# Kernel optimization log

Hardware: AMD Instinct MI355X
Metric: run time of the kernel (lower is better)

The kernel has to match this reference:

```python
import jax, jax.numpy as jnp
import numpy as np

N_WIRES = 16
VAR_DEPTH = 2
BATCH = 16


def _param_sizes():
    sizes = []
    n = N_WIRES
    lay = 0
    while n > 1:
        sizes.append(4 * int(np.ceil(N_WIRES / 2 ** lay)) * VAR_DEPTH)
        n = (n + 1) // 2
        lay += 1
    return sizes  # [128, 64, 32, 16]


def _apply_1q(psi, gate, w):
    # psi: (B, 2, ..., 2); gate: (2,2) complex; wire w lives on axis w+1
    psi = jnp.moveaxis(psi, w + 1, -1)
    psi = jnp.einsum('...j,ij->...i', psi, gate)
    return jnp.moveaxis(psi, -1, w + 1)


def _rx(psi, th, w):
    c = jnp.cos(th / 2).astype(jnp.complex64)
    s = jnp.sin(th / 2).astype(jnp.complex64)
    gate = jnp.stack([jnp.stack([c, -1j * s]), jnp.stack([-1j * s, c])])
    return _apply_1q(psi, gate, w)


def _rz(psi, th, w):
    ph = jnp.exp(0.5j * th * jnp.array([-1.0, 1.0], jnp.float32)).astype(jnp.complex64)
    shape = [1] * psi.ndim
    shape[w + 1] = 2
    return psi * ph.reshape(shape)


def _rzz(psi, th, wa, wb):
    # diag(e^{-i t/2}, e^{i t/2}, e^{i t/2}, e^{-i t/2}) -> sign = -1 if bits equal else +1
    sgn = jnp.array([[-1.0, 1.0], [1.0, -1.0]], jnp.float32)
    ph = jnp.exp(0.5j * th * sgn).astype(jnp.complex64)  # symmetric, transpose-safe
    a, b = min(wa, wb) + 1, max(wa, wb) + 1
    shape = [1] * psi.ndim
    shape[a] = 2
    shape[b] = 2
    return psi * ph.reshape(shape)


def _cnot(psi, c, t):
    p0 = jax.lax.slice_in_dim(psi, 0, 1, axis=c + 1)
    p1 = jax.lax.slice_in_dim(psi, 1, 2, axis=c + 1)
    return jnp.concatenate([p0, jnp.flip(p1, axis=t + 1)], axis=c + 1)


def _conv_layer(psi, params, active):
    n = len(active)
    for d in range(VAR_DEPTH):
        for j in range(n):
            base = 4 * j + d * 4 * n
            psi = _rx(psi, params[base + 0], active[j])
            psi = _rz(psi, params[base + 1], active[j])
            psi = _rx(psi, params[base + 2], active[j])
        for bg in (0, 1):
            for j in range(bg, n, 2):
                jn = (j + 1) % n  # ring coupling (wraps last->first)
                base = 4 * j + d * 4 * n
                psi = _rzz(psi, params[base + 3], active[j], active[jn])
    return psi


def _pool(psi, active):
    for j in range(0, len(active), 2):
        if j + 1 < len(active):
            psi = _cnot(psi, active[j], active[j + 1])
    return psi, active[::2]


def _forward(psi, params_list):
    active = list(range(N_WIRES))
    for p in params_list:
        psi = _conv_layer(psi, p, active)
        if len(active) > 1:
            psi, active = _pool(psi, active)
    w = active[0]  # measure Z on the surviving wire (wire 0)
    prob = psi.real ** 2 + psi.imag ** 2
    axes = tuple(a for a in range(1, psi.ndim) if a != w + 1)
    p2 = prob.sum(axis=axes)  # (B, 2)
    return p2[:, 0] - p2[:, 1]


def setup_inputs() -> dict:
    key = jax.random.key(0)
    ks = jax.random.split(key, 8)
    dim = 2 ** N_WIRES
    x_re = jax.random.normal(ks[0], (BATCH, dim), dtype=jnp.float32)
    x_im = jax.random.normal(ks[1], (BATCH, dim), dtype=jnp.float32)
    nrm = jnp.sqrt(jnp.sum(x_re ** 2 + x_im ** 2, axis=1, keepdims=True))
    x_re = x_re / nrm
    x_im = x_im / nrm
    sizes = _param_sizes()
    two_pi = 2.0 * np.pi
    params = [jax.random.uniform(ks[2 + i], (sizes[i],), dtype=jnp.float32) * two_pi
              for i in range(len(sizes))]
    return {"x_re": x_re, "x_im": x_im,
            "params0": params[0], "params1": params[1],
            "params2": params[2], "params3": params[3]}


def reference(x_re, x_im, params0, params1, params2, params3):
    psi = (x_re + 1j * x_im).astype(jnp.complex64)
    psi = psi.reshape((BATCH,) + (2,) * N_WIRES)
    return _forward(psi, [params0, params1, params2, params3])
```

## Files before the change

### kernel.cpp

```cpp
#include <hip/hip_runtime.h>


#define DEV __device__ __forceinline__
#define TBL(i) (tbl + (i)*8)

__device__ static const unsigned char G_CP[60] = {
  15,14,13,12,11,10,9,8,7,6,5,4,3,2,1,0,
  15,14,13,12,11,10,9,8,7,6,5,4,3,2,1,0,
  15,13,11,9,7,5,3,1,
  15,13,11,9,7,5,3,1,
  15,11,7,3,
  15,11,7,3,
  15,7,
  15,7
};
__device__ static const unsigned char G_CQ[60] = {
  14,13,12,11,10,9,8,7,6,5,4,3,2,1,0,15,
  14,13,12,11,10,9,8,7,6,5,4,3,2,1,0,15,
  13,11,9,7,5,3,1,15,
  13,11,9,7,5,3,1,15,
  11,7,3,15,
  11,7,3,15,
  7,15,
  7,15
};

DEV float2 F2(float x, float y){ float2 r; r.x = x; r.y = y; return r; }
DEV float2 cmulf(float2 a, float2 b){ return F2(a.x*b.x - a.y*b.y, a.x*b.y + a.y*b.x); }
DEV int swz(int j){ return j ^ ((j>>4)&15) ^ ((j>>8)&15); }

template<int A,int B>
DEV int mapj(int t, int s){
  int j = ((s&1)<<A) | (((s>>1)&1)<<B);
  int ti = 0;
  #pragma unroll
  for (int b=0;b<11;b++){
    if (b!=A && b!=B){ j |= ((t>>ti)&1)<<b; ti++; }
  }
  return j;
}

template<int SB>
DEV void gate4(float2* a, const float* __restrict__ g){
  float u00r=g[0],u00i=g[1],u01r=g[2],u01i=g[3],u10r=g[4],u10i=g[5],u11r=g[6],u11i=g[7];
  #pragma unroll
  for (int m=0;m<2;m++){
    int i0 = (SB==0) ? (m<<1) : m;
    int i1 = i0 | (1<<SB);
    float2 x0=a[i0], x1=a[i1];
    a[i0] = F2(u00r*x0.x - u00i*x0.y + u01r*x1.x - u01i*x1.y,
               u00r*x0.y + u00i*x0.x + u01r*x1.y + u01i*x1.x);
    a[i1] = F2(u10r*x0.x - u10i*x0.y + u11r*x1.x - u11i*x1.y,
               u10r*x0.y + u10i*x0.x + u11r*x1.y + u11i*x1.x);
  }
}

template<int C0,int N,unsigned M0,unsigned M1>
DEV void diag4(float2* a, const float* __restrict__ tbl, unsigned Ib){
  const unsigned regmask = M0|M1;
  float2 F0 = F2(1.f, 0.f);
  #pragma unroll
  for (int k=0;k<N;k++){
    const int p = G_CP[C0+k], q = G_CQ[C0+k];
    if ( !(((1u<<p)|(1u<<q)) & regmask) ){
      float c = tbl[480 + 2*(C0+k)], s = tbl[481 + 2*(C0+k)];
      unsigned x = ((Ib>>p) ^ (Ib>>q)) & 1u;
      F0 = cmulf(F0, F2(c, x ? s : -s));
    }
  }
  #pragma unroll
  for (int r=0;r<4;r++){
    unsigned Ir = Ib ^ ((r&1)?M0:0u) ^ ((r&2)?M1:0u);
    float2 ph = F0;
    #pragma unroll
    for (int k=0;k<N;k++){
      const int p = G_CP[C0+k], q = G_CQ[C0+k];
      if ( ((1u<<p)|(1u<<q)) & regmask ){
        float c = tbl[480 + 2*(C0+k)], s = tbl[481 + 2*(C0+k)];
        unsigned x = ((Ir>>p) ^ (Ir>>q)) & 1u;
        ph = cmulf(ph, F2(c, x ? s : -s));
      }
    }
    a[r] = cmulf(a[r], ph);
  }
}

DEV unsigned Ia(int j, int o){ return (unsigned)(j | (o<<11)); }
DEV unsigned Ib2(int j, int o){ return (unsigned)((j&63) | (o<<6) | ((j>>6)<<11)); }
DEV unsigned Ic(int j, int o){
  return (unsigned)( ((j&1)<<1) | (((j>>1)&1)<<3) | (((j>>2)&1)<<5)
       | (((j>>3)&63)<<6) | (((j>>9)&1)<<13) | (((j>>10)&1)<<15)
       | (o&1) | (((o>>1)&1)<<2) | (((o>>2)&1)<<4) | (((o>>3)&1)<<12) | (((o>>4)&1)<<14) );
}
DEV int s2perm(int j){ return j ^ (((j>>8)&1)<<6) ^ (((j>>4)&1)<<2) ^ (((j>>1)&1)<<0); }
DEV int s3perm(int j){ return j ^ (((j>>10)&1)<<8) ^ (((j>>4)&1)<<1); }

__global__ void k_setup(const float* __restrict__ p0, const float* __restrict__ p1,
                        const float* __restrict__ p2, const float* __restrict__ p3,
                        float* __restrict__ tbl, float* __restrict__ out){
  int g = threadIdx.x;
  if (g < 16) out[g] = 0.f;
  if (g >= 60) return;
  int d, j, n; const float* P;
  if (g < 32)      { n=16; d=(g>>4)&1; j=g&15; P=p0; }
  else if (g < 48) { n=8;  d=(g>>3)&1; j=g&7;  P=p1; }
  else if (g < 56) { n=4;  d=(g>>2)&1; j=g&3;  P=p2; }
  else             { n=2;  d=(g>>1)&1; j=g&1;  P=p3; }
  int base = 4*j + 4*n*d;
  double th0 = P[base+0], th1 = P[base+1], th2 = P[base+2], th3 = P[base+3];
  double c0 = cos(th0*0.5), s0 = sin(th0*0.5);
  double ca = cos(th1*0.5), sa = sin(th1*0.5);
  double c2 = cos(th2*0.5), s2 = sin(th2*0.5);
  double B00r =  ca*c0, B00i = -sa*c0;
  double B01r = -sa*s0, B01i = -ca*s0;
  double B10r =  sa*s0, B10i = -ca*s0;
  double B11r =  ca*c0, B11i =  sa*c0;
  float* o = tbl + g*8;
  o[0]=(float)(c2*B00r + s2*B10i); o[1]=(float)(c2*B00i - s2*B10r);
  o[2]=(float)(c2*B01r + s2*B11i); o[3]=(float)(c2*B01i - s2*B11r);
  o[4]=(float)(s2*B00i + c2*B10r); o[5]=(float)(-s2*B00r + c2*B10i);
  o[6]=(float)(s2*B01i + c2*B11r); o[7]=(float)(-s2*B01r + c2*B11i);
  tbl[480 + 2*g] = (float)cos(th3*0.5);
  tbl[481 + 2*g] = (float)sin(th3*0.5);
}

__global__ __launch_bounds__(512, 4)
void k_p1(const float* __restrict__ xre, const float* __restrict__ xim,
          const float* __restrict__ tbl, float2* __restrict__ st){
  const int t = threadIdx.x;
  const int batch = blockIdx.x >> 5, o = blockIdx.x & 31;
  const unsigned hi = ((unsigned)batch<<16) | ((unsigned)o<<11);
  __shared__ float2 lds[2][2048];
  float2 a[4];
  {
    unsigned base = hi | ((unsigned)t<<2);
    float4 re = *(const float4*)(xre + base);
    float4 im = *(const float4*)(xim + base);
    a[0]=F2(re.x,im.x); a[1]=F2(re.y,im.y); a[2]=F2(re.z,im.z); a[3]=F2(re.w,im.w);
  }
  gate4<0>(a, TBL(15)); gate4<1>(a, TBL(14));
  #pragma unroll
  for (int s=0;s<4;s++) lds[0][swz(mapj<0,1>(t,s))] = a[s];
  __syncthreads();
  #pragma unroll
  for (int s=0;s<4;s++) a[s] = lds[0][swz(mapj<2,3>(t,s))];
  gate4<0>(a, TBL(13)); gate4<1>(a, TBL(12));
  #pragma unroll
  for (int s=0;s<4;s++) lds[1][swz(mapj<2,3>(t,s))] = a[s];
  __syncthreads();
  #pragma unroll
  for (int s=0;s<4;s++) a[s] = lds[1][swz(mapj<4,5>(t,s))];
  gate4<0>(a, TBL(11)); gate4<1>(a, TBL(10));
  #pragma unroll
  for (int s=0;s<4;s++) lds[0][swz(mapj<4,5>(t,s))] = a[s];
  __syncthreads();
  #pragma unroll
  for (int s=0;s<4;s++) a[s] = lds[0][swz(mapj<6,7>(t,s))];
  gate4<0>(a, TBL(9)); gate4<1>(a, TBL(8));
  #pragma unroll
  for (int s=0;s<4;s++) lds[1][swz(mapj<6,7>(t,s))] = a[s];
  __syncthreads();
  #pragma unroll
  for (int s=0;s<4;s++) a[s] = lds[1][swz(mapj<8,9>(t,s))];
  gate4<0>(a, TBL(7)); gate4<1>(a, TBL(6));
  #pragma unroll
  for (int s=0;s<4;s++) lds[0][swz(mapj<8,9>(t,s))] = a[s];
  __syncthreads();
  #pragma unroll
  for (int s=0;s<4;s++) a[s] = lds[0][swz(mapj<0,10>(t,s))];
  gate4<1>(a, TBL(5));
  #pragma unroll
  for (int s=0;s<4;s++) st[hi | (unsigned)mapj<0,10>(t,s)] = a[s];
}

__global__ __launch_bounds__(512, 4)
void k_p2(const float* __restrict__ tbl, float2* __restrict__ st){
  const int t = threadIdx.x;
  const int batch = blockIdx.x >> 5, o = blockIdx.x & 31;
  const unsigned bb = (unsigned)batch<<16;
  __shared__ float2 lds[2][2048];
  float2 a[4];
  #pragma unroll
  for (int s=0;s<4;s++) a[s] = st[bb | Ib2(mapj<10,9>(t,s), o)];
  gate4<0>(a, TBL(0)); gate4<1>(a, TBL(1));
  #pragma unroll
  for (int s=0;s<4;s++) lds[0][swz(mapj<10,9>(t,s))] = a[s];
  __syncthreads();
  #pragma unroll
  for (int s=0;s<4;s++) a[s] = lds[0][swz(mapj<8,7>(t,s))];
  gate4<0>(a, TBL(2)); gate4<1>(a, TBL(3));
  #pragma unroll
  for (int s=0;s<4;s++) lds[1][swz(mapj<8,7>(t,s))] = a[s];
  __syncthreads();
  #pragma unroll
  for (int s=0;s<4;s++) a[s] = lds[1][swz(mapj<6,5>(t,s))];
  gate4<0>(a, TBL(4));
  diag4<0,16, (1u<<11),(1u<<5)>(a, tbl, Ib2(mapj<6,5>(t,0), o));
  gate4<0>(a, TBL(20)); gate4<1>(a, TBL(26));
  #pragma unroll
  for (int s=0;s<4;s++) lds[0][swz(mapj<6,5>(t,s))] = a[s];
  __syncthreads();
  #pragma unroll
  for (int s=0;s<4;s++) a[s] = lds[0][swz(mapj<7,8>(t,s))];
  gate4<0>(a, TBL(19)); gate4<1>(a, TBL(18));
  #pragma unroll
  for (int s=0;s<4;s++) lds[1][swz(mapj<7,8>(t,s))] = a[s];
  __syncthreads();
  #pragma unroll
  for (int s=0;s<4;s++) a[s] = lds[1][swz(mapj<9,10>(t,s))];
  gate4<0>(a, TBL(17)); gate4<1>(a, TBL(16));
  #pragma unroll
  for (int s=0;s<4;s++) lds[0][swz(mapj<9,10>(t,s))] = a[s];
  __syncthreads();
  #pragma unroll
  for (int s=0;s<4;s++) a[s] = lds[0][swz(mapj<0,1>(t,s))];
  gate4<0>(a, TBL(31)); gate4<1>(a, TBL(30));
  #pragma unroll
  for (int s=0;s<4;s++) lds[1][swz(mapj<0,1>(t,s))] = a[s];
  __syncthreads();
  #pragma unroll
  for (int s=0;s<4;s++) a[s] = lds[1][swz(mapj<2,3>(t,s))];
  gate4<0>(a, TBL(29)); gate4<1>(a, TBL(28));
  #pragma unroll
  for (int s=0;s<4;s++) lds[0][swz(mapj<2,3>(t,s))] = a[s];
  __syncthreads();
  #pragma unroll
  for (int s=0;s<4;s++) a[s] = lds[0][swz(mapj<4,10>(t,s))];
  gate4<0>(a, TBL(27));
  #pragma unroll
  for (int s=0;s<4;s++) st[bb | Ib2(mapj<4,10>(t,s), o)] = a[s];
}

__global__ __launch_bounds__(512, 4)
void k_p3(const float* __restrict__ tbl, float2* __restrict__ st){
  const int t = threadIdx.x;
  const int batch = blockIdx.x >> 5, o = blockIdx.x & 31;
  const unsigned hi = ((unsigned)batch<<16) | ((unsigned)o<<11);
  __shared__ float2 lds[2][2048];
  float2 a[4];
  #pragma unroll
  for (int s=0;s<4;s++) a[s] = st[hi | (unsigned)mapj<6,7>(t,s)];
  gate4<0>(a, TBL(25)); gate4<1>(a, TBL(24));
  #pragma unroll
  for (int s=0;s<4;s++) lds[0][swz(mapj<6,7>(t,s))] = a[s];
  __syncthreads();
  #pragma unroll
  for (int s=0;s<4;s++) a[s] = lds[0][swz(mapj<8,9>(t,s))];
  gate4<0>(a, TBL(23)); gate4<1>(a, TBL(22));
  #pragma unroll
  for (int s=0;s<4;s++) lds[1][swz(mapj<8,9>(t,s))] = a[s];
  __syncthreads();
  #pragma unroll
  for (int s=0;s<4;s++) a[s] = lds[1][swz(mapj<0,10>(t,s))];
  gate4<1>(a, TBL(21));
  diag4<16,16, 1u,(1u<<10)>(a, tbl, Ia(mapj<0,10>(t,0), o));
  #pragma unroll
  for (int s=0;s<4;s++) st[hi | (unsigned)mapj<0,10>(t,s)] = a[s];
}

__global__ __launch_bounds__(512, 4)
void k_p4(const float* __restrict__ tbl, float2* __restrict__ st, float* __restrict__ out){
  const int t = threadIdx.x;
  const int batch = blockIdx.x >> 5, o = blockIdx.x & 31;
  const unsigned bb = (unsigned)batch<<16;
  __shared__ float2 lds[2][2048];
  __shared__ float red[8];
  float2 a[4];
  #pragma unroll
  for (int s=0;s<4;s++){
    unsigned I = Ic(mapj<10,9>(t,s), o);
    I ^= (I & 0xAAAAu) >> 1;
    a[s] = st[bb | I];
  }
  gate4<0>(a, TBL(32)); gate4<1>(a, TBL(33));
  #pragma unroll
  for (int s=0;s<4;s++) lds[0][swz(mapj<10,9>(t,s))] = a[s];
  __syncthreads();
  #pragma unroll
  for (int s=0;s<4;s++) a[s] = lds[0][swz(mapj<8,6>(t,s))];
  gate4<0>(a, TBL(34)); gate4<1>(a, TBL(35));
  #pragma unroll
  for (int s=0;s<4;s++) lds[1][swz(mapj<8,6>(t,s))] = a[s];
  __syncthreads();
  #pragma unroll
  for (int s=0;s<4;s++) a[s] = lds[1][swz(mapj<4,2>(t,s))];
  gate4<0>(a, TBL(36)); gate4<1>(a, TBL(37));
  #pragma unroll
  for (int s=0;s<4;s++) lds[0][swz(mapj<4,2>(t,s))] = a[s];
  __syncthreads();
  #pragma unroll
  for (int s=0;s<4;s++) a[s] = lds[0][swz(mapj<1,0>(t,s))];
  gate4<0>(a, TBL(38)); gate4<1>(a, TBL(39));
  diag4<32,8, (1u<<3),(1u<<1)>(a, tbl, Ic(mapj<1,0>(t,0), o));
  gate4<0>(a, TBL(46)); gate4<1>(a, TBL(47));
  #pragma unroll
  for (int s=0;s<4;s++) lds[1][swz(mapj<1,0>(t,s))] = a[s];
  __syncthreads();
  #pragma unroll
  for (int s=0;s<4;s++) a[s] = lds[1][swz(mapj<2,4>(t,s))];
  gate4<0>(a, TBL(45)); gate4<1>(a, TBL(44));
  #pragma unroll
  for (int s=0;s<4;s++) lds[0][swz(mapj<2,4>(t,s))] = a[s];
  __syncthreads();
  #pragma unroll
  for (int s=0;s<4;s++) a[s] = lds[0][swz(mapj<6,8>(t,s))];
  gate4<0>(a, TBL(43)); gate4<1>(a, TBL(42));
  #pragma unroll
  for (int s=0;s<4;s++) lds[1][swz(mapj<6,8>(t,s))] = a[s];
  __syncthreads();
  #pragma unroll
  for (int s=0;s<4;s++) a[s] = lds[1][swz(mapj<9,10>(t,s))];
  gate4<0>(a, TBL(41)); gate4<1>(a, TBL(40));
  diag4<40,8, (1u<<13),(1u<<15)>(a, tbl, Ic(mapj<9,10>(t,0), o));
  { float2 tmp=a[2]; a[2]=a[3]; a[3]=tmp; }
  gate4<1>(a, TBL(48));
  #pragma unroll
  for (int s=0;s<4;s++) lds[0][swz(mapj<9,10>(t,s))] = a[s];
  __syncthreads();
  #pragma unroll
  for (int s=0;s<4;s++) a[s] = lds[0][swz(s2perm(mapj<8,4>(t,s)))];
  gate4<0>(a, TBL(49)); gate4<1>(a, TBL(50));
  #pragma unroll
  for (int s=0;s<4;s++) lds[1][swz(mapj<8,4>(t,s))] = a[s];
  __syncthreads();
  #pragma unroll
  for (int s=0;s<4;s++) a[s] = lds[1][swz(mapj<1,10>(t,s))];
  gate4<0>(a, TBL(51));
  diag4<48,4, (1u<<3),(1u<<15)>(a, tbl, Ic(mapj<1,10>(t,0), o));
  gate4<0>(a, TBL(55)); gate4<1>(a, TBL(52));
  #pragma unroll
  for (int s=0;s<4;s++) lds[0][swz(mapj<1,10>(t,s))] = a[s];
  __syncthreads();
  #pragma unroll
  for (int s=0;s<4;s++) a[s] = lds[0][swz(mapj<4,8>(t,s))];
  gate4<0>(a, TBL(54)); gate4<1>(a, TBL(53));
  diag4<52,4, (1u<<7),(1u<<11)>(a, tbl, Ic(mapj<4,8>(t,0), o));
  #pragma unroll
  for (int s=0;s<4;s++) lds[1][swz(mapj<4,8>(t,s))] = a[s];
  __syncthreads();
  #pragma unroll
  for (int s=0;s<4;s++) a[s] = lds[1][swz(s3perm(mapj<4,10>(t,s)))];
  gate4<0>(a, TBL(57)); gate4<1>(a, TBL(56));
  diag4<56,2, (1u<<7),(1u<<15)>(a, tbl, Ic(mapj<4,10>(t,0), o));
  gate4<1>(a, TBL(58));
  float s = 0.f;
  #pragma unroll
  for (int r=0;r<4;r++){
    float w = a[r].x*a[r].x + a[r].y*a[r].y;
    s += (r & 2) ? -w : w;
  }
  #pragma unroll
  for (int off=32; off>0; off>>=1) s += __shfl_down(s, off);
  if ((t & 63) == 0) red[t>>6] = s;
  __syncthreads();
  if (t == 0){
    float tot = 0.f;
    #pragma unroll
    for (int w=0; w<8; w++) tot += red[w];
    atomicAdd(out + batch, tot);
  }
}

extern "C" void kernel_launch(void* const* d_in, const int* in_sizes, int n_in,
                              void* d_out, int out_size, void* d_ws, size_t ws_size,
                              hipStream_t stream) {
  const float* xre = (const float*)d_in[0];
  const float* xim = (const float*)d_in[1];
  const float* p0  = (const float*)d_in[2];
  const float* p1  = (const float*)d_in[3];
  const float* p2  = (const float*)d_in[4];
  const float* p3  = (const float*)d_in[5];
  float* out = (float*)d_out;
  float2* st = (float2*)d_ws;
  float* tbl = (float*)((char*)d_ws + (8u<<20));

  k_setup<<<1, 64, 0, stream>>>(p0, p1, p2, p3, tbl, out);
  k_p1<<<512, 512, 0, stream>>>(xre, xim, tbl, st);
  k_p2<<<512, 512, 0, stream>>>(tbl, st);
  k_p3<<<512, 512, 0, stream>>>(tbl, st);
  k_p4<<<512, 512, 0, stream>>>(tbl, st, out);
}
```

Before: 114.3 us.

## Apply gates via wavefront shuffles and merge p3 into neighbouring passes

Replaces most shared-memory transposes between gate pairs with in-register gates that exchange amplitudes across lanes using __shfl_xor. Each pass now needs only one LDS round trip. The qubit-to-thread mapping is reorganised so the former third pass folds into the other kernels, removing one full read and write of the global state and one launch. In exchange, each gate costs more cross-lane shuffles and selects, and the hand-built bit mappings are easy to get wrong.

Measured after the change: 114.0 us. No clear change (-0.2%).

```diff
diff --git a/kernel.cpp b/kernel.cpp
--- a/kernel.cpp
+++ b/kernel.cpp
@@ -29,17 +29,6 @@
 DEV float2 cmulf(float2 a, float2 b){ return F2(a.x*b.x - a.y*b.y, a.x*b.y + a.y*b.x); }
 DEV int swz(int j){ return j ^ ((j>>4)&15) ^ ((j>>8)&15); }
 
-template<int A,int B>
-DEV int mapj(int t, int s){
-  int j = ((s&1)<<A) | (((s>>1)&1)<<B);
-  int ti = 0;
-  #pragma unroll
-  for (int b=0;b<11;b++){
-    if (b!=A && b!=B){ j |= ((t>>ti)&1)<<b; ti++; }
-  }
-  return j;
-}
-
 template<int SB>
 DEV void gate4(float2* a, const float* __restrict__ g){
   float u00r=g[0],u00i=g[1],u01r=g[2],u01i=g[3],u10r=g[4],u10i=g[5],u11r=g[6],u11i=g[7];
@@ -52,6 +41,31 @@
                u00r*x0.y + u00i*x0.x + u01r*x1.y + u01i*x1.x);
     a[i1] = F2(u10r*x0.x - u10i*x0.y + u11r*x1.x - u11i*x1.y,
                u10r*x0.y + u10i*x0.x + u11r*x1.y + u11i*x1.x);
+  }
+}
+
+DEV void lgate(float2* a, const float* __restrict__ g, int mask, int lane){
+  bool h = (lane & mask) != 0;
+  float c0r = h ? g[4] : g[0], c0i = h ? g[5] : g[1];
+  float c1r = h ? g[6] : g[2], c1i = h ? g[7] : g[3];
+  #pragma unroll
+  for (int s=0;s<4;s++){
+    float px = __shfl_xor(a[s].x, mask);
+    float py = __shfl_xor(a[s].y, mask);
+    float x0x = h ? px : a[s].x, x0y = h ? py : a[s].y;
+    float x1x = h ? a[s].x : px, x1y = h ? a[s].y : py;
+    a[s] = F2(c0r*x0x - c0i*x0y + c1r*x1x - c1i*x1y,
+              c0r*x0y + c0i*x0x + c1r*x1y + c1i*x1x);
+  }
+}
+
+DEV void cswap(float2* a, int cmask, int tmask, int lane){
+  bool c = (lane & cmask) != 0;
+  #pragma unroll
+  for (int s=0;s<4;s++){
+    float px = __shfl_xor(a[s].x, tmask);
+    float py = __shfl_xor(a[s].y, tmask);
+    if (c){ a[s].x = px; a[s].y = py; }
   }
 }
 
@@ -85,15 +99,13 @@
   }
 }
 
-DEV unsigned Ia(int j, int o){ return (unsigned)(j | (o<<11)); }
 DEV unsigned Ib2(int j, int o){ return (unsigned)((j&63) | (o<<6) | ((j>>6)<<11)); }
 DEV unsigned Ic(int j, int o){
   return (unsigned)( ((j&1)<<1) | (((j>>1)&1)<<3) | (((j>>2)&1)<<5)
        | (((j>>3)&63)<<6) | (((j>>9)&1)<<13) | (((j>>10)&1)<<15)
        | (o&1) | (((o>>1)&1)<<2) | (((o>>2)&1)<<4) | (((o>>3)&1)<<12) | (((o>>4)&1)<<14) );
 }
-DEV int s2perm(int j){ return j ^ (((j>>8)&1)<<6) ^ (((j>>4)&1)<<2) ^ (((j>>1)&1)<<0); }
-DEV int s3perm(int j){ return j ^ (((j>>10)&1)<<8) ^ (((j>>4)&1)<<1); }
+DEV unsigned s1b(unsigned I){ return I ^ ((I & 0xA02Au) >> 1); }
 
 __global__ void k_setup(const float* __restrict__ p0, const float* __restrict__ p1,
                         const float* __restrict__ p2, const float* __restrict__ p3,
@@ -127,10 +139,10 @@
 __global__ __launch_bounds__(512, 4)
 void k_p1(const float* __restrict__ xre, const float* __restrict__ xim,
           const float* __restrict__ tbl, float2* __restrict__ st){
-  const int t = threadIdx.x;
+  const int t = threadIdx.x, lane = t & 63, wv = t >> 6;
   const int batch = blockIdx.x >> 5, o = blockIdx.x & 31;
   const unsigned hi = ((unsigned)batch<<16) | ((unsigned)o<<11);
-  __shared__ float2 lds[2][2048];
+  __shared__ float2 lds[2048];
   float2 a[4];
   {
     unsigned base = hi | ((unsigned)t<<2);
@@ -139,219 +151,135 @@
     a[0]=F2(re.x,im.x); a[1]=F2(re.y,im.y); a[2]=F2(re.z,im.z); a[3]=F2(re.w,im.w);
   }
   gate4<0>(a, TBL(15)); gate4<1>(a, TBL(14));
-  #pragma unroll
-  for (int s=0;s<4;s++) lds[0][swz(mapj<0,1>(t,s))] = a[s];
-  __syncthreads();
-  #pragma unroll
-  for (int s=0;s<4;s++) a[s] = lds[0][swz(mapj<2,3>(t,s))];
-  gate4<0>(a, TBL(13)); gate4<1>(a, TBL(12));
-  #pragma unroll
-  for (int s=0;s<4;s++) lds[1][swz(mapj<2,3>(t,s))] = a[s];
-  __syncthreads();
-  #pragma unroll
-  for (int s=0;s<4;s++) a[s] = lds[1][swz(mapj<4,5>(t,s))];
-  gate4<0>(a, TBL(11)); gate4<1>(a, TBL(10));
-  #pragma unroll
-  for (int s=0;s<4;s++) lds[0][swz(mapj<4,5>(t,s))] = a[s];
-  __syncthreads();
-  #pragma unroll
-  for (int s=0;s<4;s++) a[s] = lds[0][swz(mapj<6,7>(t,s))];
-  gate4<0>(a, TBL(9)); gate4<1>(a, TBL(8));
-  #pragma unroll
-  for (int s=0;s<4;s++) lds[1][swz(mapj<6,7>(t,s))] = a[s];
-  __syncthreads();
-  #pragma unroll
-  for (int s=0;s<4;s++) a[s] = lds[1][swz(mapj<8,9>(t,s))];
+  lgate(a, TBL(13), 1, lane);  lgate(a, TBL(12), 2, lane);
+  lgate(a, TBL(11), 4, lane);  lgate(a, TBL(10), 8, lane);
+  lgate(a, TBL(9), 16, lane);  lgate(a, TBL(8), 32, lane);
+  #pragma unroll
+  for (int s=0;s<4;s++) lds[swz((t<<2)|s)] = a[s];
+  __syncthreads();
+  #pragma unroll
+  for (int s=0;s<4;s++){
+    int jB = (lane&31) | (wv<<5) | (s<<8) | ((lane>>5)<<10);
+    a[s] = lds[swz(jB)];
+  }
   gate4<0>(a, TBL(7)); gate4<1>(a, TBL(6));
-  #pragma unroll
-  for (int s=0;s<4;s++) lds[0][swz(mapj<8,9>(t,s))] = a[s];
-  __syncthreads();
-  #pragma unroll
-  for (int s=0;s<4;s++) a[s] = lds[0][swz(mapj<0,10>(t,s))];
-  gate4<1>(a, TBL(5));
-  #pragma unroll
-  for (int s=0;s<4;s++) st[hi | (unsigned)mapj<0,10>(t,s)] = a[s];
+  lgate(a, TBL(5), 32, lane);
+  #pragma unroll
+  for (int s=0;s<4;s++){
+    int jB = (lane&31) | (wv<<5) | (s<<8) | ((lane>>5)<<10);
+    st[hi | (unsigned)jB] = a[s];
+  }
 }
 
 __global__ __launch_bounds__(512, 4)
 void k_p2(const float* __restrict__ tbl, float2* __restrict__ st){
-  const int t = threadIdx.x;
+  const int t = threadIdx.x, lane = t & 63, wv = t >> 6;
   const int batch = blockIdx.x >> 5, o = blockIdx.x & 31;
   const unsigned bb = (unsigned)batch<<16;
-  __shared__ float2 lds[2][2048];
+  __shared__ float2 lds[2048];
   float2 a[4];
-  #pragma unroll
-  for (int s=0;s<4;s++) a[s] = st[bb | Ib2(mapj<10,9>(t,s), o)];
+  int jA0 = ((lane&1)<<8) | (((lane>>1)&1)<<7) | (((lane>>2)&1)<<6)
+          | (((lane>>3)&1)<<0) | (((lane>>4)&1)<<1) | (((lane>>5)&1)<<2) | (wv<<3);
+  #pragma unroll
+  for (int s=0;s<4;s++){
+    int jA = jA0 | ((s&1)<<10) | (((s>>1)&1)<<9);
+    a[s] = st[bb | Ib2(jA, o)];
+  }
   gate4<0>(a, TBL(0)); gate4<1>(a, TBL(1));
-  #pragma unroll
-  for (int s=0;s<4;s++) lds[0][swz(mapj<10,9>(t,s))] = a[s];
-  __syncthreads();
-  #pragma unroll
-  for (int s=0;s<4;s++) a[s] = lds[0][swz(mapj<8,7>(t,s))];
-  gate4<0>(a, TBL(2)); gate4<1>(a, TBL(3));
-  #pragma unroll
-  for (int s=0;s<4;s++) lds[1][swz(mapj<8,7>(t,s))] = a[s];
-  __syncthreads();
-  #pragma unroll
-  for (int s=0;s<4;s++) a[s] = lds[1][swz(mapj<6,5>(t,s))];
-  gate4<0>(a, TBL(4));
-  diag4<0,16, (1u<<11),(1u<<5)>(a, tbl, Ib2(mapj<6,5>(t,0), o));
-  gate4<0>(a, TBL(20)); gate4<1>(a, TBL(26));
-  #pragma unroll
-  for (int s=0;s<4;s++) lds[0][swz(mapj<6,5>(t,s))] = a[s];
-  __syncthreads();
-  #pragma unroll
-  for (int s=0;s<4;s++) a[s] = lds[0][swz(mapj<7,8>(t,s))];
-  gate4<0>(a, TBL(19)); gate4<1>(a, TBL(18));
-  #pragma unroll
-  for (int s=0;s<4;s++) lds[1][swz(mapj<7,8>(t,s))] = a[s];
-  __syncthreads();
-  #pragma unroll
-  for (int s=0;s<4;s++) a[s] = lds[1][swz(mapj<9,10>(t,s))];
-  gate4<0>(a, TBL(17)); gate4<1>(a, TBL(16));
-  #pragma unroll
-  for (int s=0;s<4;s++) lds[0][swz(mapj<9,10>(t,s))] = a[s];
-  __syncthreads();
-  #pragma unroll
-  for (int s=0;s<4;s++) a[s] = lds[0][swz(mapj<0,1>(t,s))];
-  gate4<0>(a, TBL(31)); gate4<1>(a, TBL(30));
-  #pragma unroll
-  for (int s=0;s<4;s++) lds[1][swz(mapj<0,1>(t,s))] = a[s];
-  __syncthreads();
-  #pragma unroll
-  for (int s=0;s<4;s++) a[s] = lds[1][swz(mapj<2,3>(t,s))];
-  gate4<0>(a, TBL(29)); gate4<1>(a, TBL(28));
-  #pragma unroll
-  for (int s=0;s<4;s++) lds[0][swz(mapj<2,3>(t,s))] = a[s];
-  __syncthreads();
-  #pragma unroll
-  for (int s=0;s<4;s++) a[s] = lds[0][swz(mapj<4,10>(t,s))];
-  gate4<0>(a, TBL(27));
-  #pragma unroll
-  for (int s=0;s<4;s++) st[bb | Ib2(mapj<4,10>(t,s), o)] = a[s];
-}
-
-__global__ __launch_bounds__(512, 4)
-void k_p3(const float* __restrict__ tbl, float2* __restrict__ st){
-  const int t = threadIdx.x;
-  const int batch = blockIdx.x >> 5, o = blockIdx.x & 31;
-  const unsigned hi = ((unsigned)batch<<16) | ((unsigned)o<<11);
-  __shared__ float2 lds[2][2048];
-  float2 a[4];
-  #pragma unroll
-  for (int s=0;s<4;s++) a[s] = st[hi | (unsigned)mapj<6,7>(t,s)];
-  gate4<0>(a, TBL(25)); gate4<1>(a, TBL(24));
-  #pragma unroll
-  for (int s=0;s<4;s++) lds[0][swz(mapj<6,7>(t,s))] = a[s];
-  __syncthreads();
-  #pragma unroll
-  for (int s=0;s<4;s++) a[s] = lds[0][swz(mapj<8,9>(t,s))];
-  gate4<0>(a, TBL(23)); gate4<1>(a, TBL(22));
-  #pragma unroll
-  for (int s=0;s<4;s++) lds[1][swz(mapj<8,9>(t,s))] = a[s];
-  __syncthreads();
-  #pragma unroll
-  for (int s=0;s<4;s++) a[s] = lds[1][swz(mapj<0,10>(t,s))];
-  gate4<1>(a, TBL(21));
-  diag4<16,16, 1u,(1u<<10)>(a, tbl, Ia(mapj<0,10>(t,0), o));
-  #pragma unroll
-  for (int s=0;s<4;s++) st[hi | (unsigned)mapj<0,10>(t,s)] = a[s];
+  lgate(a, TBL(2), 1, lane); lgate(a, TBL(3), 2, lane); lgate(a, TBL(4), 4, lane);
+  diag4<0,16, (1u<<15),(1u<<14)>(a, tbl, Ib2(jA0, o));
+  lgate(a, TBL(20), 4, lane); lgate(a, TBL(19), 2, lane); lgate(a, TBL(18), 1, lane);
+  gate4<1>(a, TBL(17)); gate4<0>(a, TBL(16));
+  lgate(a, TBL(31), 8, lane); lgate(a, TBL(30), 16, lane); lgate(a, TBL(29), 32, lane);
+  #pragma unroll
+  for (int s=0;s<4;s++){
+    int jA = jA0 | ((s&1)<<10) | (((s>>1)&1)<<9);
+    lds[swz(jA)] = a[s];
+  }
+  __syncthreads();
+  int jB0 = (lane&7) | (((lane>>3)&1)<<5) | (wv<<6)
+          | (((lane>>4)&1)<<9) | (((lane>>5)&1)<<10);
+  #pragma unroll
+  for (int s=0;s<4;s++){
+    int jB = jB0 | ((s&1)<<3) | (((s>>1)&1)<<4);
+    a[s] = lds[swz(jB)];
+  }
+  gate4<0>(a, TBL(28)); gate4<1>(a, TBL(27));
+  lgate(a, TBL(26), 8, lane);
+  #pragma unroll
+  for (int s=0;s<4;s++){
+    int jB = jB0 | ((s&1)<<3) | (((s>>1)&1)<<4);
+    st[bb | Ib2(jB, o)] = a[s];
+  }
 }
 
 __global__ __launch_bounds__(512, 4)
 void k_p4(const float* __restrict__ tbl, float2* __restrict__ st, float* __restrict__ out){
-  const int t = threadIdx.x;
+  const int t = threadIdx.x, lane = t & 63, wv = t >> 6;
   const int batch = blockIdx.x >> 5, o = blockIdx.x & 31;
   const unsigned bb = (unsigned)batch<<16;
-  __shared__ float2 lds[2][2048];
+  __shared__ float2 lds[2048];
   __shared__ float red[8];
   float2 a[4];
-  #pragma unroll
-  for (int s=0;s<4;s++){
-    unsigned I = Ic(mapj<10,9>(t,s), o);
-    I ^= (I & 0xAAAAu) >> 1;
-    a[s] = st[bb | I];
-  }
-  gate4<0>(a, TBL(32)); gate4<1>(a, TBL(33));
-  #pragma unroll
-  for (int s=0;s<4;s++) lds[0][swz(mapj<10,9>(t,s))] = a[s];
-  __syncthreads();
-  #pragma unroll
-  for (int s=0;s<4;s++) a[s] = lds[0][swz(mapj<8,6>(t,s))];
-  gate4<0>(a, TBL(34)); gate4<1>(a, TBL(35));
-  #pragma unroll
-  for (int s=0;s<4;s++) lds[1][swz(mapj<8,6>(t,s))] = a[s];
-  __syncthreads();
-  #pragma unroll
-  for (int s=0;s<4;s++) a[s] = lds[1][swz(mapj<4,2>(t,s))];
-  gate4<0>(a, TBL(36)); gate4<1>(a, TBL(37));
-  #pragma unroll
-  for (int s=0;s<4;s++) lds[0][swz(mapj<4,2>(t,s))] = a[s];
-  __syncthreads();
-  #pragma unroll
-  for (int s=0;s<4;s++) a[s] = lds[0][swz(mapj<1,0>(t,s))];
-  gate4<0>(a, TBL(38)); gate4<1>(a, TBL(39));
-  diag4<32,8, (1u<<3),(1u<<1)>(a, tbl, Ic(mapj<1,0>(t,0), o));
-  gate4<0>(a, TBL(46)); gate4<1>(a, TBL(47));
-  #pragma unroll
-  for (int s=0;s<4;s++) lds[1][swz(mapj<1,0>(t,s))] = a[s];
-  __syncthreads();
-  #pragma unroll
-  for (int s=0;s<4;s++) a[s] = lds[1][swz(mapj<2,4>(t,s))];
-  gate4<0>(a, TBL(45)); gate4<1>(a, TBL(44));
-  #pragma unroll
-  for (int s=0;s<4;s++) lds[0][swz(mapj<2,4>(t,s))] = a[s];
-  __syncthreads();
-  #pragma unroll
-  for (int s=0;s<4;s++) a[s] = lds[0][swz(mapj<6,8>(t,s))];
-  gate4<0>(a, TBL(43)); gate4<1>(a, TBL(42));
-  #pragma unroll
-  for (int s=0;s<4;s++) lds[1][swz(mapj<6,8>(t,s))] = a[s];
-  __syncthreads();
-  #pragma unroll
-  for (int s=0;s<4;s++) a[s] = lds[1][swz(mapj<9,10>(t,s))];
-  gate4<0>(a, TBL(41)); gate4<1>(a, TBL(40));
-  diag4<40,8, (1u<<13),(1u<<15)>(a, tbl, Ic(mapj<9,10>(t,0), o));
+  int jA0 = (lane&7) | (((lane>>3)&7)<<5) | (wv<<8);
+  #pragma unroll
+  for (int s=0;s<4;s++){
+    int jA = jA0 | ((s&1)<<3) | (((s>>1)&1)<<4);
+    a[s] = st[bb | s1b(Ic(jA, o))];
+  }
+  gate4<0>(a, TBL(25)); gate4<1>(a, TBL(24));
+  lgate(a, TBL(23), 8, lane); lgate(a, TBL(22), 16, lane); lgate(a, TBL(21), 32, lane);
+  diag4<16,16, (1u<<6),(1u<<7)>(a, tbl, s1b(Ic(jA0, o)));
+  if (wv & 1){
+    #pragma unroll
+    for (int s=0;s<4;s++){ a[s].x = __shfl_xor(a[s].x, 32); a[s].y = __shfl_xor(a[s].y, 32); }
+  }
+  cswap(a, 16, 8, lane);
   { float2 tmp=a[2]; a[2]=a[3]; a[3]=tmp; }
-  gate4<1>(a, TBL(48));
-  #pragma unroll
-  for (int s=0;s<4;s++) lds[0][swz(mapj<9,10>(t,s))] = a[s];
-  __syncthreads();
-  #pragma unroll
-  for (int s=0;s<4;s++) a[s] = lds[0][swz(s2perm(mapj<8,4>(t,s)))];
-  gate4<0>(a, TBL(49)); gate4<1>(a, TBL(50));
-  #pragma unroll
-  for (int s=0;s<4;s++) lds[1][swz(mapj<8,4>(t,s))] = a[s];
-  __syncthreads();
-  #pragma unroll
-  for (int s=0;s<4;s++) a[s] = lds[1][swz(mapj<1,10>(t,s))];
-  gate4<0>(a, TBL(51));
-  diag4<48,4, (1u<<3),(1u<<15)>(a, tbl, Ic(mapj<1,10>(t,0), o));
-  gate4<0>(a, TBL(55)); gate4<1>(a, TBL(52));
-  #pragma unroll
-  for (int s=0;s<4;s++) lds[0][swz(mapj<1,10>(t,s))] = a[s];
-  __syncthreads();
-  #pragma unroll
-  for (int s=0;s<4;s++) a[s] = lds[0][swz(mapj<4,8>(t,s))];
-  gate4<0>(a, TBL(54)); gate4<1>(a, TBL(53));
-  diag4<52,4, (1u<<7),(1u<<11)>(a, tbl, Ic(mapj<4,8>(t,0), o));
-  #pragma unroll
-  for (int s=0;s<4;s++) lds[1][swz(mapj<4,8>(t,s))] = a[s];
-  __syncthreads();
-  #pragma unroll
-  for (int s=0;s<4;s++) a[s] = lds[1][swz(s3perm(mapj<4,10>(t,s)))];
-  gate4<0>(a, TBL(57)); gate4<1>(a, TBL(56));
-  diag4<56,2, (1u<<7),(1u<<15)>(a, tbl, Ic(mapj<4,10>(t,0), o));
-  gate4<1>(a, TBL(58));
-  float s = 0.f;
-  #pragma unroll
-  for (int r=0;r<4;r++){
-    float w = a[r].x*a[r].x + a[r].y*a[r].y;
-    s += (r & 2) ? -w : w;
-  }
-  #pragma unroll
-  for (int off=32; off>0; off>>=1) s += __shfl_down(s, off);
-  if ((t & 63) == 0) red[t>>6] = s;
+  #pragma unroll
+  for (int s=0;s<4;s++){
+    int jA = jA0 | ((s&1)<<3) | (((s>>1)&1)<<4);
+    lds[swz(jA)] = a[s];
+  }
+  __syncthreads();
+  int jB0 = ((lane&1)<<2) | (((lane>>1)&1)<<4) | (((lane>>2)&1)<<6)
+          | (((lane>>3)&1)<<8) | (((lane>>4)&1)<<9) | (((lane>>5)&1)<<10)
+          | ((wv&1)<<3) | (((wv>>1)&1)<<5) | (((wv>>2)&1)<<7);
+  #pragma unroll
+  for (int s=0;s<4;s++) a[s] = lds[swz(jB0 | (s&1) | (((s>>1)&1)<<1))];
+  const unsigned IbB = Ic(jB0, o);
+  gate4<0>(a, TBL(39)); gate4<1>(a, TBL(38));
+  lgate(a, TBL(37), 1, lane); lgate(a, TBL(36), 2, lane); lgate(a, TBL(35), 4, lane);
+  lgate(a, TBL(34), 8, lane); lgate(a, TBL(33), 16, lane); lgate(a, TBL(32), 32, lane);
+  diag4<32,8, 2u,8u>(a, tbl, IbB);
+  gate4<0>(a, TBL(47)); gate4<1>(a, TBL(46));
+  lgate(a, TBL(45), 1, lane); lgate(a, TBL(44), 2, lane); lgate(a, TBL(43), 4, lane);
+  lgate(a, TBL(42), 8, lane); lgate(a, TBL(41), 16, lane); lgate(a, TBL(40), 32, lane);
+  diag4<40,8, 2u,8u>(a, tbl, IbB);
+  cswap(a, 32, 16, lane); cswap(a, 8, 4, lane); cswap(a, 2, 1, lane);
+  { float2 tmp=a[2]; a[2]=a[3]; a[3]=tmp; }
+  lgate(a, TBL(48), 32, lane); lgate(a, TBL(49), 8, lane); lgate(a, TBL(50), 2, lane);
+  gate4<1>(a, TBL(51));
+  diag4<48,4, 2u,8u>(a, tbl, IbB);
+  lgate(a, TBL(52), 32, lane); lgate(a, TBL(53), 8, lane); lgate(a, TBL(54), 2, lane);
+  gate4<1>(a, TBL(55));
+  diag4<52,4, 2u,8u>(a, tbl, IbB);
+  cswap(a, 32, 8, lane);
+  if (lane & 2){
+    float2 t0=a[0]; a[0]=a[2]; a[2]=t0;
+    float2 t1=a[1]; a[1]=a[3]; a[3]=t1;
+  }
+  lgate(a, TBL(56), 32, lane); lgate(a, TBL(57), 2, lane);
+  diag4<56,2, 2u,8u>(a, tbl, IbB);
+  lgate(a, TBL(58), 32, lane);
+  float sl = 0.f;
+  #pragma unroll
+  for (int s=0;s<4;s++) sl += a[s].x*a[s].x + a[s].y*a[s].y;
+  float sg = (lane & 32) ? -sl : sl;
+  #pragma unroll
+  for (int off=32; off>0; off>>=1) sg += __shfl_down(sg, off);
+  __syncthreads();
+  if ((t & 63) == 0) red[wv] = sg;
   __syncthreads();
   if (t == 0){
     float tot = 0.f;
@@ -377,6 +305,5 @@
   k_setup<<<1, 64, 0, stream>>>(p0, p1, p2, p3, tbl, out);
   k_p1<<<512, 512, 0, stream>>>(xre, xim, tbl, st);
   k_p2<<<512, 512, 0, stream>>>(tbl, st);
-  k_p3<<<512, 512, 0, stream>>>(tbl, st);
   k_p4<<<512, 512, 0, stream>>>(tbl, st, out);
 }
```
